# Kernel optimization log

Hardware: AMD Instinct MI355X
Metric: run time of the kernel (lower is better)

The kernel has to match this reference:

```python
import jax, jax.numpy as jnp
import numpy as np

HEADS = 8
NEG = -1e9
EPS = 1e-9


def setup_inputs() -> dict:
    key = jax.random.key(0)
    ks = jax.random.split(key, 24)
    N, D, E = 2048, 512, 64
    s = 0.02
    inp = {
        "xyz": jax.random.normal(ks[0], (N, 3), jnp.float32),
        "str_feat": jax.random.normal(ks[1], (N, D), jnp.float32),
        "esm_feat": jax.random.normal(ks[2], (N, E), jnp.float32),
        "y_hat": jax.random.uniform(ks[3], (N, 1), jnp.float32),
        "distance_mask": jax.random.randint(ks[4], (N, N), 0, 2, jnp.int32),
        "t": jnp.ones((1,), jnp.float32),
        "band_width": jnp.ones((1,), jnp.float32),
        "max_iter": 5,
        # main projections (torch Linear layout: y = x @ W.T + b)
        "Wq": jax.random.normal(ks[5], (D, D), jnp.float32) * s,
        "bq": jnp.zeros((D,), jnp.float32),
        "Wk": jax.random.normal(ks[6], (D, D), jnp.float32) * s,
        "bk": jnp.zeros((D,), jnp.float32),
        "Wv": jax.random.normal(ks[7], (D, D), jnp.float32) * s,
        "bv": jnp.zeros((D,), jnp.float32),
        "Wo": jax.random.normal(ks[8], (D, D), jnp.float32) * s,
        "bo": jnp.zeros((D,), jnp.float32),
        # esm projections (computed in the original forward but unused downstream)
        "Weq": jax.random.normal(ks[9], (E, E), jnp.float32) * s,
        "beq": jnp.zeros((E,), jnp.float32),
        "Wek": jax.random.normal(ks[10], (E, E), jnp.float32) * s,
        "bek": jnp.zeros((E,), jnp.float32),
        "Wev": jax.random.normal(ks[11], (E, E), jnp.float32) * s,
        "bev": jnp.zeros((E,), jnp.float32),
        "Weo": jax.random.normal(ks[12], (E, E), jnp.float32) * s,
        "beo": jnp.zeros((E,), jnp.float32),
    }
    return inp


def reference(xyz, str_feat, esm_feat, y_hat, distance_mask, t, band_width, max_iter,
              Wq, bq, Wk, bk, Wv, bv, Wo, bo,
              Weq, beq, Wek, bek, Wev, bev, Weo, beo):
    N, D = str_feat.shape
    h = HEADS
    dh = D // h

    q = str_feat @ Wq.T + bq
    k = str_feat @ Wk.T + bk
    v = str_feat @ Wv.T + bv
    # esm projections: computed in the original forward but never used (dead code; DCE'd under jit)
    _esm_q = esm_feat @ Weq.T + beq
    _esm_k = esm_feat @ Wek.T + bek
    _esm_v = esm_feat @ Wev.T + bev

    # [h, N, dh]
    qh = q.reshape(N, h, dh).transpose(1, 0, 2)
    kh = k.reshape(N, h, dh).transpose(1, 0, 2)
    vh = v.reshape(N, h, dh).transpose(1, 0, 2)

    scores = jnp.einsum('hnd,hmd->hnm', qh, kh) / jnp.sqrt(jnp.asarray(dh, qh.dtype))
    mask = (distance_mask > 0)[None]              # [1, N, N]
    yw = y_hat[:, 0][None, :]                     # [1, N] per-target weight
    inv_two_bw2 = 1.0 / (2.0 * band_width[0] ** 2)
    temp = t[0]

    def step(carry, _):
        xyz_c, _x = carry
        # squared pairwise distances via the expanded form (avoids [N,N,3])
        sq = jnp.sum(xyz_c * xyz_c, axis=-1)
        d2 = sq[:, None] + sq[None, :] - 2.0 * (xyz_c @ xyz_c.T)
        kern = jnp.exp(-d2 * inv_two_bw2)          # [N, N] band-width kernel
        logits = scores / temp + jnp.log(kern * yw + EPS)[None]
        logits = jnp.where(mask, logits, NEG)
        attn = jax.nn.softmax(logits, axis=-1)     # [h, N, N]
        xyz_new = jnp.einsum('nm,md->nd', attn.mean(0), xyz_c)  # mean-shift step
        x_new = jnp.einsum('hnm,hmd->hnd', attn, vh)            # [h, N, dh]
        return (xyz_new, x_new), None

    (xyz_out, xh), _ = jax.lax.scan(step, (xyz, jnp.zeros_like(vh)), None, length=max_iter)
    x = xh.transpose(1, 0, 2).reshape(N, D)
    out = x @ Wo.T + bo
    return xyz_out, out
```

## Files before the change

### kernel.cpp

```cpp
#include <hip/hip_runtime.h>


typedef __attribute__((ext_vector_type(8))) short bf16x8;
typedef __attribute__((ext_vector_type(4))) float f32x4;

__device__ __forceinline__ unsigned short f2bf(float f) {
    unsigned int u = __float_as_uint(f);
    u += 0x7fff + ((u >> 16) & 1);
    return (unsigned short)(u >> 16);
}
__device__ __forceinline__ float bf2f(unsigned short u) {
    return __uint_as_float((unsigned int)u << 16);
}

union EU { bf16x8 v; unsigned short u[8]; };

__global__ __launch_bounds__(256)
void conv_all(const float* __restrict__ strf,
              const float* __restrict__ Wq, const float* __restrict__ Wk,
              const float* __restrict__ Wv, const float* __restrict__ Wo,
              const int* __restrict__ dmask,
              unsigned short* __restrict__ sA, unsigned short* __restrict__ sW,
              unsigned char* __restrict__ mby)
{
    const long base = (long)(blockIdx.x * 256 + threadIdx.x) * 8;
    if (base >= 2097152) {
        const long rel = base - 2097152;
        int4 a = *reinterpret_cast<const int4*>(dmask + rel);
        int4 b = *reinterpret_cast<const int4*>(dmask + rel + 4);
        unsigned long long p = 0;
        p |= (a.x > 0) ? 0x01ULL : 0;  p |= (a.y > 0) ? 0x0100ULL : 0;
        p |= (a.z > 0) ? 0x010000ULL : 0;  p |= (a.w > 0) ? 0x01000000ULL : 0;
        p |= (b.x > 0) ? 0x0100000000ULL : 0;  p |= (b.y > 0) ? 0x010000000000ULL : 0;
        p |= (b.z > 0) ? 0x01000000000000ULL : 0;  p |= (b.w > 0) ? 0x0100000000000000ULL : 0;
        *reinterpret_cast<unsigned long long*>(mby + rel) = p;
        return;
    }
    const float* src;
    unsigned short* dst;
    if (base < 1048576) {
        src = strf + base; dst = sA + base;
    } else {
        const long rel = base - 1048576;
        const int seg = (int)(rel >> 18);
        const long off = rel & 262143;
        const float* Ws[4] = {Wq, Wk, Wv, Wo};
        src = Ws[seg] + off;
        dst = sW + (long)seg * 262144 + off;
    }
    float4 a = *reinterpret_cast<const float4*>(src);
    float4 b = *reinterpret_cast<const float4*>(src + 4);
    EU o;
    o.u[0] = f2bf(a.x); o.u[1] = f2bf(a.y); o.u[2] = f2bf(a.z); o.u[3] = f2bf(a.w);
    o.u[4] = f2bf(b.x); o.u[5] = f2bf(b.y); o.u[6] = f2bf(b.z); o.u[7] = f2bf(b.w);
    *reinterpret_cast<bf16x8*>(dst) = o.v;
}

__global__ __launch_bounds__(256)
void qkv_mfma(const unsigned short* __restrict__ sA,
              const unsigned short* __restrict__ sW,
              const float* __restrict__ bq, const float* __restrict__ bk,
              const float* __restrict__ bv,
              unsigned short* __restrict__ qh, unsigned short* __restrict__ kh,
              unsigned short* __restrict__ vT)
{
    const int z  = blockIdx.z;
    const int bx = blockIdx.x;
    const int by = blockIdx.y;
    const int tid = threadIdx.x;
    const int wv = tid >> 6;
    const int lane = tid & 63;
    const int row  = lane & 15;
    const int koct = (lane >> 4) * 8;
    const int n0 = bx * 64;

    const unsigned short* Ap = sA + (long)(n0 + wv * 16 + row) * 512;
    const unsigned short* Bp = sW + (long)z * 262144 + (long)(by * 64 + row) * 512;

    f32x4 acc[4] = {};
#pragma unroll
    for (int k0 = 0; k0 < 512; k0 += 32) {
        bf16x8 a = *reinterpret_cast<const bf16x8*>(Ap + k0 + koct);
#pragma unroll
        for (int t = 0; t < 4; t++) {
            bf16x8 b = *reinterpret_cast<const bf16x8*>(Bp + (long)(t * 16) * 512 + k0 + koct);
            acc[t] = __builtin_amdgcn_mfma_f32_16x16x32_bf16(a, b, acc[t], 0, 0, 0);
        }
    }

    if (z == 2) {
        const int rbase = n0 + wv * 16 + (lane >> 4) * 4;
#pragma unroll
        for (int t = 0; t < 4; t++) {
            const int d = by * 64 + t * 16 + (lane & 15);
            const float bb = bv[d];
            ushort4 o;
            o.x = f2bf(acc[t][0] + bb); o.y = f2bf(acc[t][1] + bb);
            o.z = f2bf(acc[t][2] + bb); o.w = f2bf(acc[t][3] + bb);
            *reinterpret_cast<ushort4*>(vT + (long)d * 2048 + rbase) = o;
        }
        return;
    }

    __shared__ float ls[64][68];
    const int lrb = wv * 16 + (lane >> 4) * 4;
    const int lcb = lane & 15;
#pragma unroll
    for (int t = 0; t < 4; t++)
#pragma unroll
        for (int r = 0; r < 4; r++)
            ls[lrb + r][t * 16 + lcb] = acc[t][r];
    __syncthreads();

    const float* bias = (z == 0) ? bq : bk;
    unsigned short* dst = (z == 0) ? qh : kh;
    const int r2 = tid >> 2;
    const int c2 = (tid & 3) * 16;
    float sv[16];
#pragma unroll
    for (int j = 0; j < 4; j++) {
        float4 s = *reinterpret_cast<const float4*>(&ls[r2][c2 + j * 4]);
        float4 bb = *reinterpret_cast<const float4*>(bias + by * 64 + c2 + j * 4);
        sv[j*4+0] = s.x + bb.x; sv[j*4+1] = s.y + bb.y;
        sv[j*4+2] = s.z + bb.z; sv[j*4+3] = s.w + bb.w;
    }
    EU o0, o1;
#pragma unroll
    for (int j = 0; j < 8; j++) { o0.u[j] = f2bf(sv[j]); o1.u[j] = f2bf(sv[8 + j]); }
    unsigned short* dp = dst + (long)(n0 + r2) * 512 + by * 64 + c2;
    *reinterpret_cast<bf16x8*>(dp)     = o0.v;
    *reinterpret_cast<bf16x8*>(dp + 8) = o1.v;
}

__global__ __launch_bounds__(256)
void scores_rows(const unsigned short* __restrict__ qh,
                 const unsigned short* __restrict__ kh,
                 const unsigned char* __restrict__ mby,
                 const float* __restrict__ tptr,
                 unsigned short* __restrict__ Ebf)
{
    const int h  = blockIdx.y;
    const int n0 = blockIdx.x * 16;
    const int tid = threadIdx.x;
    const int wv = tid >> 6;
    const int lane = tid & 63;
    const float scale = 1.0f / (8.0f * tptr[0]);

    __shared__ unsigned short lsb[4][16][260];

    const int arow = lane & 15;
    const int koct = (lane >> 4) * 8;
    const unsigned short* Aq = qh + (long)(n0 + arow) * 512 + h * 64;
    const bf16x8 aq0 = *reinterpret_cast<const bf16x8*>(Aq + koct);
    const bf16x8 aq1 = *reinterpret_cast<const bf16x8*>(Aq + 32 + koct);

    const int lr = (lane >> 4) * 4;
    const int lc = lane & 15;
    const int rlo = lane >> 5;
    const int cch = lane & 31;

#pragma unroll
    for (int half = 0; half < 2; half++) {
        const int mbase = wv * 512 + half * 256;
#pragma unroll
        for (int mt = 0; mt < 16; mt++) {
            const unsigned short* Bk = kh + (long)(mbase + mt * 16 + arow) * 512 + h * 64;
            bf16x8 b0 = *reinterpret_cast<const bf16x8*>(Bk + koct);
            bf16x8 b1 = *reinterpret_cast<const bf16x8*>(Bk + 32 + koct);
            f32x4 c = {};
            c = __builtin_amdgcn_mfma_f32_16x16x32_bf16(aq0, b0, c, 0, 0, 0);
            c = __builtin_amdgcn_mfma_f32_16x16x32_bf16(aq1, b1, c, 0, 0, 0);
#pragma unroll
            for (int r = 0; r < 4; r++)
                lsb[wv][lr + r][mt * 16 + lc] = f2bf(__expf(c[r] * scale));
        }
#pragma unroll
        for (int rp = 0; rp < 8; rp++) {
            const int row = rp * 2 + rlo;
            const int gn = n0 + row;
            const int m = mbase + cch * 8;
            EU e;
            e.v = *reinterpret_cast<const bf16x8*>(&lsb[wv][row][cch * 8]);
            unsigned long long mk =
                *reinterpret_cast<const unsigned long long*>(mby + (long)gn * 2048 + m);
            EU o;
#pragma unroll
            for (int j = 0; j < 8; j++)
                o.u[j] = ((mk >> (8 * j)) & 0xff) ? e.u[j] : (unsigned short)0;
            *reinterpret_cast<bf16x8*>(Ebf + ((long)h * 2048 + gn) * 2048 + m) = o.v;
        }
    }
}

__global__ __launch_bounds__(256)
void ms_iter(const unsigned short* __restrict__ Ebf,
             const float* __restrict__ xyz_src,
             float* __restrict__ xyz_dst,
             const float* __restrict__ y_hat,
             const float* __restrict__ bwp,
             unsigned short* __restrict__ gbf,
             float* __restrict__ invzb,
             int wlast)
{
    const int n = blockIdx.x;
    const int tid = threadIdx.x;
    const int lane = tid & 63;
    const int wave = tid >> 6;
    const int m0 = tid * 8;

    __shared__ unsigned short Es[8][4][512];
    __shared__ float red[64];

    {
        const unsigned short* gp = Ebf + (long)n * 2048 + wave * 512 + lane * 8;
#pragma unroll
        for (int h = 0; h < 8; h++) {
            __builtin_amdgcn_global_load_lds(
                (const __attribute__((address_space(1))) unsigned int*)(gp + (long)h * 4194304),
                (__attribute__((address_space(3))) unsigned int*)&Es[h][wave][0],
                16, 0, 0);
        }
    }

    const float bw = bwp[0];
    const float c2k = 1.0f / (2.0f * bw * bw);
    const float xn = xyz_src[n * 3 + 0];
    const float yn = xyz_src[n * 3 + 1];
    const float zn = xyz_src[n * 3 + 2];
    const float sqn = xn * xn + yn * yn + zn * zn;

    float mx[8], my[8], mz[8];
    {
        const float4* xp = reinterpret_cast<const float4*>(xyz_src + (long)m0 * 3);
        float4 a = xp[0], b = xp[1], c = xp[2], d = xp[3], e = xp[4], f = xp[5];
        mx[0]=a.x; my[0]=a.y; mz[0]=a.z;  mx[1]=a.w; my[1]=b.x; mz[1]=b.y;
        mx[2]=b.z; my[2]=b.w; mz[2]=c.x;  mx[3]=c.y; my[3]=c.z; mz[3]=c.w;
        mx[4]=d.x; my[4]=d.y; mz[4]=d.z;  mx[5]=d.w; my[5]=e.x; mz[5]=e.y;
        mx[6]=e.z; my[6]=e.w; mz[6]=f.x;  mx[7]=f.y; my[7]=f.z; mz[7]=f.w;
    }
    float4 yh0 = *reinterpret_cast<const float4*>(y_hat + m0);
    float4 yh1 = *reinterpret_cast<const float4*>(y_hat + m0 + 4);
    float yh[8] = {yh0.x, yh0.y, yh0.z, yh0.w, yh1.x, yh1.y, yh1.z, yh1.w};

    float g[8];
#pragma unroll
    for (int j = 0; j < 8; j++) {
        const float d2 = sqn + (mx[j]*mx[j] + my[j]*my[j] + mz[j]*mz[j])
                       - 2.0f * (xn*mx[j] + yn*my[j] + zn*mz[j]);
        g[j] = __expf(-d2 * c2k) * yh[j] + 1e-9f;
    }

    __syncthreads();

    EU E[8];
#pragma unroll
    for (int h = 0; h < 8; h++)
        E[h].v = *reinterpret_cast<const bf16x8*>(&Es[h][wave][lane * 8]);

    float z[8];
#pragma unroll
    for (int h = 0; h < 8; h++) {
        float zz = 0.f;
#pragma unroll
        for (int j = 0; j < 8; j++) zz += bf2f(E[h].u[j]) * g[j];
        z[h] = zz;
    }

#pragma unroll
    for (int h = 0; h < 8; h++) {
        float v = z[h];
#pragma unroll
        for (int off = 32; off > 0; off >>= 1) v += __shfl_down(v, off, 64);
        if (lane == 0) red[wave * 8 + h] = v;
    }
    __syncthreads();
    if (tid < 8) {
        const float s = red[tid] + red[8 + tid] + red[16 + tid] + red[24 + tid];
        const float iz = 1.0f / s;
        red[32 + tid] = iz;
        if (wlast) invzb[tid * 2048 + n] = iz;
    }
    __syncthreads();
    float invz[8];
#pragma unroll
    for (int h = 0; h < 8; h++) invz[h] = red[32 + h];

    float ax = 0.f, ay = 0.f, az = 0.f;
#pragma unroll
    for (int j = 0; j < 8; j++) {
        float w = 0.f;
#pragma unroll
        for (int h = 0; h < 8; h++) w += bf2f(E[h].u[j]) * invz[h];
        w *= 0.125f * g[j];
        ax += w * mx[j]; ay += w * my[j]; az += w * mz[j];
    }
    if (wlast) {
        EU og;
#pragma unroll
        for (int j = 0; j < 8; j++) og.u[j] = f2bf(g[j]);
        *reinterpret_cast<bf16x8*>(gbf + (long)n * 2048 + m0) = og.v;
    }

    float v3[3] = {ax, ay, az};
#pragma unroll
    for (int c = 0; c < 3; c++) {
        float v = v3[c];
#pragma unroll
        for (int off = 32; off > 0; off >>= 1) v += __shfl_down(v, off, 64);
        if (lane == 0) red[40 + c * 4 + wave] = v;
    }
    __syncthreads();
    if (tid < 3) {
        xyz_dst[n * 3 + tid] = red[40 + tid * 4 + 0] + red[40 + tid * 4 + 1] +
                               red[40 + tid * 4 + 2] + red[40 + tid * 4 + 3];
    }
}

__global__ __launch_bounds__(256)
void av_mfma(const unsigned short* __restrict__ Ebf,
             const unsigned short* __restrict__ gbf,
             const unsigned short* __restrict__ vT,
             float* __restrict__ P)
{
    const int h  = blockIdx.z;
    const int s  = blockIdx.y;
    const int bx = blockIdx.x;
    const int tid = threadIdx.x;
    const int wv = tid >> 6;
    const int lane = tid & 63;
    const int n0 = bx * 64;
    const int kc = s * 512;

    __shared__ unsigned short As[64][132];

    const int mrow = lane & 15;
    const int koct = (lane >> 4) * 8;
    const int srow = tid >> 4;
    const int skk  = (tid & 15) * 8;

    f32x4 acc[4] = {};
    for (int kt = 0; kt < 4; kt++) {
        const int kb = kc + kt * 128;
        __syncthreads();
#pragma unroll
        for (int l = 0; l < 4; l++) {
            const int row = l * 16 + srow;
            EU e, gg;
            e.v  = *reinterpret_cast<const bf16x8*>(Ebf + ((long)h * 2048 + n0 + row) * 2048 + kb + skk);
            gg.v = *reinterpret_cast<const bf16x8*>(gbf + (long)(n0 + row) * 2048 + kb + skk);
            EU a;
#pragma unroll
            for (int j = 0; j < 8; j++)
                a.u[j] = f2bf(bf2f(e.u[j]) * bf2f(gg.u[j]));
            *reinterpret_cast<bf16x8*>(&As[row][skk]) = a.v;
        }
        __syncthreads();
#pragma unroll
        for (int k2 = 0; k2 < 128; k2 += 32) {
            bf16x8 a = *reinterpret_cast<const bf16x8*>(&As[wv * 16 + mrow][k2 + koct]);
#pragma unroll
            for (int t = 0; t < 4; t++) {
                bf16x8 b = *reinterpret_cast<const bf16x8*>(
                    vT + ((long)h * 64 + t * 16 + mrow) * 2048 + kb + k2 + koct);
                acc[t] = __builtin_amdgcn_mfma_f32_16x16x32_bf16(a, b, acc[t], 0, 0, 0);
            }
        }
    }

    float* Pp = P + (long)s * 1048576;
    const int rbase = n0 + wv * 16 + (lane >> 4) * 4;
    const int dcol = lane & 15;
#pragma unroll
    for (int t = 0; t < 4; t++)
#pragma unroll
        for (int r = 0; r < 4; r++)
            Pp[(long)(rbase + r) * 512 + h * 64 + t * 16 + dcol] = acc[t][r];
}

__global__ __launch_bounds__(256)
void av_red(const float* __restrict__ P, const float* __restrict__ invzb,
            unsigned short* __restrict__ xc)
{
    const long idx = (long)(blockIdx.x * 256 + threadIdx.x) * 8;
    const int n = (int)(idx >> 9);
    const int d0 = (int)(idx & 511);
    const float iz = invzb[(d0 >> 6) * 2048 + n];
    float s[8] = {};
#pragma unroll
    for (int p = 0; p < 4; p++) {
        const float* pp = P + (long)p * 1048576 + idx;
        float4 a = *reinterpret_cast<const float4*>(pp);
        float4 b = *reinterpret_cast<const float4*>(pp + 4);
        s[0] += a.x; s[1] += a.y; s[2] += a.z; s[3] += a.w;
        s[4] += b.x; s[5] += b.y; s[6] += b.z; s[7] += b.w;
    }
    EU o;
#pragma unroll
    for (int j = 0; j < 8; j++) o.u[j] = f2bf(s[j] * iz);
    *reinterpret_cast<bf16x8*>(xc + idx) = o.v;
}

__global__ __launch_bounds__(256)
void out_mfma(const unsigned short* __restrict__ xc,
              const unsigned short* __restrict__ sW,
              const float* __restrict__ bo,
              float* __restrict__ out)
{
    const int bx = blockIdx.x;
    const int by = blockIdx.y;
    const int wv = threadIdx.x >> 6;
    const int lane = threadIdx.x & 63;
    const int row  = lane & 15;
    const int koct = (lane >> 4) * 8;
    const int n0 = bx * 64;

    const unsigned short* Ap = xc + (long)(n0 + wv * 16 + row) * 512;
    const unsigned short* Bp = sW + 3L * 262144 + (long)(by * 64 + row) * 512;

    f32x4 acc[4] = {};
#pragma unroll
    for (int k0 = 0; k0 < 512; k0 += 32) {
        bf16x8 a = *reinterpret_cast<const bf16x8*>(Ap + k0 + koct);
#pragma unroll
        for (int t = 0; t < 4; t++) {
            bf16x8 b = *reinterpret_cast<const bf16x8*>(Bp + (long)(t * 16) * 512 + k0 + koct);
            acc[t] = __builtin_amdgcn_mfma_f32_16x16x32_bf16(a, b, acc[t], 0, 0, 0);
        }
    }

    const int rbase = n0 + wv * 16 + (lane >> 4) * 4;
    const int dcol = lane & 15;
#pragma unroll
    for (int t = 0; t < 4; t++) {
        const int col = by * 64 + t * 16 + dcol;
        const float bb = bo[col];
#pragma unroll
        for (int r = 0; r < 4; r++)
            out[(long)(rbase + r) * 512 + col] = acc[t][r] + bb;
    }
}

extern "C" void kernel_launch(void* const* d_in, const int* in_sizes, int n_in,
                              void* d_out, int out_size, void* d_ws, size_t ws_size,
                              hipStream_t stream)
{
    (void)in_sizes; (void)n_in; (void)out_size; (void)ws_size;

    const float* xyz   = (const float*)d_in[0];
    const float* strf  = (const float*)d_in[1];
    const float* yhat  = (const float*)d_in[3];
    const int*   dmask = (const int*)d_in[4];
    const float* tptr  = (const float*)d_in[5];
    const float* bwptr = (const float*)d_in[6];
    const float* Wq = (const float*)d_in[8];
    const float* bq = (const float*)d_in[9];
    const float* Wk = (const float*)d_in[10];
    const float* bk = (const float*)d_in[11];
    const float* Wv = (const float*)d_in[12];
    const float* bv = (const float*)d_in[13];
    const float* Wo = (const float*)d_in[14];
    const float* bo = (const float*)d_in[15];
    float* outp = (float*)d_out;

    char* wsb = (char*)d_ws;
    float* Ppart         = (float*)(wsb);
    unsigned short* xc   = (unsigned short*)(wsb + (16L << 20));
    unsigned short* sA   = (unsigned short*)(wsb + (18L << 20));
    unsigned short* sW   = (unsigned short*)(wsb + (20L << 20));
    unsigned short* qh   = (unsigned short*)(wsb + (22L << 20));
    unsigned short* kh   = (unsigned short*)(wsb + (24L << 20));
    unsigned short* vT   = (unsigned short*)(wsb + (26L << 20));
    float* xyzA          = (float*)(wsb + (28L << 20));
    float* xyzB          = xyzA + 8192;
    unsigned char* mby   = (unsigned char*)(wsb + (30L << 20));
    unsigned short* Ebf  = (unsigned short*)(wsb + (34L << 20));
    unsigned short* gbf  = (unsigned short*)(wsb + (98L << 20));
    float* invzb         = (float*)(wsb + (106L << 20));

    dim3 blk(256, 1, 1);

    conv_all<<<dim3(3072), blk, 0, stream>>>(strf, Wq, Wk, Wv, Wo, dmask, sA, sW, mby);
    qkv_mfma<<<dim3(32, 8, 3), blk, 0, stream>>>(sA, sW, bq, bk, bv, qh, kh, vT);

    scores_rows<<<dim3(128, 8), blk, 0, stream>>>(qh, kh, mby, tptr, Ebf);

    const float* src = xyz;
    float* dsts[5] = {xyzA, xyzB, xyzA, xyzB, outp};
    for (int it = 0; it < 5; it++) {
        ms_iter<<<dim3(2048), blk, 0, stream>>>(Ebf, src, dsts[it], yhat, bwptr,
                                                gbf, invzb, it == 4 ? 1 : 0);
        src = dsts[it];
    }

    av_mfma<<<dim3(32, 4, 8), blk, 0, stream>>>(Ebf, gbf, vT, Ppart);
    av_red<<<dim3(512), blk, 0, stream>>>(Ppart, invzb, xc);
    out_mfma<<<dim3(32, 8), blk, 0, stream>>>(xc, sW, bo, outp + 6144);
}
```

Measured before the change: 315.1 us.

## Split score kernel over grid z and double-buffer rows in mean-shift kernel

The score kernel now launches a third grid dimension for the two column halves, which doubles the block count, and it preloads the mask words before the MFMA loop. The mean-shift iteration kernel handles four query rows per block instead of one. It double-buffers the per-head E rows into LDS through async global_load_lds, controlled by explicit vmcnt waits, and computes per-column squared norms once. This is meant to hide global load latency and amortise xyz/y_hat loads. The cost is fewer blocks (512) and hand-written waitcnt/barrier code, which is fragile and could hurt occupancy.

```diff
diff --git a/kernel.cpp b/kernel.cpp
--- a/kernel.cpp
+++ b/kernel.cpp
@@ -139,10 +139,11 @@
                  const float* __restrict__ tptr,
                  unsigned short* __restrict__ Ebf)
 {
-    const int h  = blockIdx.y;
-    const int n0 = blockIdx.x * 16;
-    const int tid = threadIdx.x;
-    const int wv = tid >> 6;
+    const int h    = blockIdx.y;
+    const int n0   = blockIdx.x * 16;
+    const int half = blockIdx.z;
+    const int tid  = threadIdx.x;
+    const int wv   = tid >> 6;
     const int lane = tid & 63;
     const float scale = 1.0f / (8.0f * tptr[0]);
 
@@ -150,45 +151,47 @@
 
     const int arow = lane & 15;
     const int koct = (lane >> 4) * 8;
+    const int mbase = wv * 512 + half * 256;
+    const int rlo = lane >> 5;
+    const int cch = lane & 31;
+
+    unsigned long long mk[8];
+#pragma unroll
+    for (int rp = 0; rp < 8; rp++)
+        mk[rp] = *reinterpret_cast<const unsigned long long*>(
+            mby + (long)(n0 + rp * 2 + rlo) * 2048 + mbase + cch * 8);
+
     const unsigned short* Aq = qh + (long)(n0 + arow) * 512 + h * 64;
     const bf16x8 aq0 = *reinterpret_cast<const bf16x8*>(Aq + koct);
     const bf16x8 aq1 = *reinterpret_cast<const bf16x8*>(Aq + 32 + koct);
 
     const int lr = (lane >> 4) * 4;
     const int lc = lane & 15;
-    const int rlo = lane >> 5;
-    const int cch = lane & 31;
-
-#pragma unroll
-    for (int half = 0; half < 2; half++) {
-        const int mbase = wv * 512 + half * 256;
-#pragma unroll
-        for (int mt = 0; mt < 16; mt++) {
-            const unsigned short* Bk = kh + (long)(mbase + mt * 16 + arow) * 512 + h * 64;
-            bf16x8 b0 = *reinterpret_cast<const bf16x8*>(Bk + koct);
-            bf16x8 b1 = *reinterpret_cast<const bf16x8*>(Bk + 32 + koct);
-            f32x4 c = {};
-            c = __builtin_amdgcn_mfma_f32_16x16x32_bf16(aq0, b0, c, 0, 0, 0);
-            c = __builtin_amdgcn_mfma_f32_16x16x32_bf16(aq1, b1, c, 0, 0, 0);
-#pragma unroll
-            for (int r = 0; r < 4; r++)
-                lsb[wv][lr + r][mt * 16 + lc] = f2bf(__expf(c[r] * scale));
-        }
-#pragma unroll
-        for (int rp = 0; rp < 8; rp++) {
-            const int row = rp * 2 + rlo;
-            const int gn = n0 + row;
-            const int m = mbase + cch * 8;
-            EU e;
-            e.v = *reinterpret_cast<const bf16x8*>(&lsb[wv][row][cch * 8]);
-            unsigned long long mk =
-                *reinterpret_cast<const unsigned long long*>(mby + (long)gn * 2048 + m);
-            EU o;
-#pragma unroll
-            for (int j = 0; j < 8; j++)
-                o.u[j] = ((mk >> (8 * j)) & 0xff) ? e.u[j] : (unsigned short)0;
-            *reinterpret_cast<bf16x8*>(Ebf + ((long)h * 2048 + gn) * 2048 + m) = o.v;
-        }
+
+#pragma unroll
+    for (int mt = 0; mt < 16; mt++) {
+        const unsigned short* Bk = kh + (long)(mbase + mt * 16 + arow) * 512 + h * 64;
+        bf16x8 b0 = *reinterpret_cast<const bf16x8*>(Bk + koct);
+        bf16x8 b1 = *reinterpret_cast<const bf16x8*>(Bk + 32 + koct);
+        f32x4 c = {};
+        c = __builtin_amdgcn_mfma_f32_16x16x32_bf16(aq0, b0, c, 0, 0, 0);
+        c = __builtin_amdgcn_mfma_f32_16x16x32_bf16(aq1, b1, c, 0, 0, 0);
+#pragma unroll
+        for (int r = 0; r < 4; r++)
+            lsb[wv][lr + r][mt * 16 + lc] = f2bf(__expf(c[r] * scale));
+    }
+
+#pragma unroll
+    for (int rp = 0; rp < 8; rp++) {
+        const int row = rp * 2 + rlo;
+        EU e;
+        e.v = *reinterpret_cast<const bf16x8*>(&lsb[wv][row][cch * 8]);
+        EU o;
+#pragma unroll
+        for (int j = 0; j < 8; j++)
+            o.u[j] = ((mk[rp] >> (8 * j)) & 0xff) ? e.u[j] : (unsigned short)0;
+        *reinterpret_cast<bf16x8*>(
+            Ebf + ((long)h * 2048 + n0 + row) * 2048 + mbase + cch * 8) = o.v;
     }
 }
 
@@ -202,34 +205,34 @@
              float* __restrict__ invzb,
              int wlast)
 {
-    const int n = blockIdx.x;
-    const int tid = threadIdx.x;
+    const int tid  = threadIdx.x;
     const int lane = tid & 63;
     const int wave = tid >> 6;
-    const int m0 = tid * 8;
-
-    __shared__ unsigned short Es[8][4][512];
+    const int m0   = tid * 8;
+    const int nb   = blockIdx.x * 4;
+
+    __shared__ unsigned short Es[2][8][4][512];
     __shared__ float red[64];
 
-    {
-        const unsigned short* gp = Ebf + (long)n * 2048 + wave * 512 + lane * 8;
-#pragma unroll
-        for (int h = 0; h < 8; h++) {
-            __builtin_amdgcn_global_load_lds(
-                (const __attribute__((address_space(1))) unsigned int*)(gp + (long)h * 4194304),
-                (__attribute__((address_space(3))) unsigned int*)&Es[h][wave][0],
-                16, 0, 0);
-        }
-    }
+    const unsigned short* gp0 = Ebf + (long)nb * 2048 + wave * 512 + lane * 8;
+
+#pragma unroll
+    for (int h = 0; h < 8; h++)
+        __builtin_amdgcn_global_load_lds(
+            (const __attribute__((address_space(1))) unsigned int*)(gp0 + (long)h * 4194304),
+            (__attribute__((address_space(3))) unsigned int*)&Es[0][h][wave][0],
+            16, 0, 0);
 
     const float bw = bwp[0];
     const float c2k = 1.0f / (2.0f * bw * bw);
-    const float xn = xyz_src[n * 3 + 0];
-    const float yn = xyz_src[n * 3 + 1];
-    const float zn = xyz_src[n * 3 + 2];
-    const float sqn = xn * xn + yn * yn + zn * zn;
-
-    float mx[8], my[8], mz[8];
+    float4 rA = *reinterpret_cast<const float4*>(xyz_src + nb * 3);
+    float4 rB = *reinterpret_cast<const float4*>(xyz_src + nb * 3 + 4);
+    float4 rC = *reinterpret_cast<const float4*>(xyz_src + nb * 3 + 8);
+    const float rx[4] = {rA.x, rA.w, rB.z, rC.y};
+    const float ry[4] = {rA.y, rB.x, rB.w, rC.z};
+    const float rz[4] = {rA.z, rB.y, rC.x, rC.w};
+
+    float mx[8], my[8], mz[8], sqm[8], yh[8];
     {
         const float4* xp = reinterpret_cast<const float4*>(xyz_src + (long)m0 * 3);
         float4 a = xp[0], b = xp[1], c = xp[2], d = xp[3], e = xp[4], f = xp[5];
@@ -237,82 +240,112 @@
         mx[2]=b.z; my[2]=b.w; mz[2]=c.x;  mx[3]=c.y; my[3]=c.z; mz[3]=c.w;
         mx[4]=d.x; my[4]=d.y; mz[4]=d.z;  mx[5]=d.w; my[5]=e.x; mz[5]=e.y;
         mx[6]=e.z; my[6]=e.w; mz[6]=f.x;  mx[7]=f.y; my[7]=f.z; mz[7]=f.w;
-    }
-    float4 yh0 = *reinterpret_cast<const float4*>(y_hat + m0);
-    float4 yh1 = *reinterpret_cast<const float4*>(y_hat + m0 + 4);
-    float yh[8] = {yh0.x, yh0.y, yh0.z, yh0.w, yh1.x, yh1.y, yh1.z, yh1.w};
-
-    float g[8];
-#pragma unroll
-    for (int j = 0; j < 8; j++) {
-        const float d2 = sqn + (mx[j]*mx[j] + my[j]*my[j] + mz[j]*mz[j])
-                       - 2.0f * (xn*mx[j] + yn*my[j] + zn*mz[j]);
-        g[j] = __expf(-d2 * c2k) * yh[j] + 1e-9f;
-    }
-
-    __syncthreads();
-
-    EU E[8];
+        float4 y0 = *reinterpret_cast<const float4*>(y_hat + m0);
+        float4 y1 = *reinterpret_cast<const float4*>(y_hat + m0 + 4);
+        yh[0]=y0.x; yh[1]=y0.y; yh[2]=y0.z; yh[3]=y0.w;
+        yh[4]=y1.x; yh[5]=y1.y; yh[6]=y1.z; yh[7]=y1.w;
+#pragma unroll
+        for (int j = 0; j < 8; j++)
+            sqm[j] = mx[j]*mx[j] + my[j]*my[j] + mz[j]*mz[j];
+    }
+
 #pragma unroll
     for (int h = 0; h < 8; h++)
-        E[h].v = *reinterpret_cast<const bf16x8*>(&Es[h][wave][lane * 8]);
-
-    float z[8];
-#pragma unroll
-    for (int h = 0; h < 8; h++) {
-        float zz = 0.f;
-#pragma unroll
-        for (int j = 0; j < 8; j++) zz += bf2f(E[h].u[j]) * g[j];
-        z[h] = zz;
-    }
-
-#pragma unroll
-    for (int h = 0; h < 8; h++) {
-        float v = z[h];
-#pragma unroll
-        for (int off = 32; off > 0; off >>= 1) v += __shfl_down(v, off, 64);
-        if (lane == 0) red[wave * 8 + h] = v;
-    }
-    __syncthreads();
-    if (tid < 8) {
-        const float s = red[tid] + red[8 + tid] + red[16 + tid] + red[24 + tid];
-        const float iz = 1.0f / s;
-        red[32 + tid] = iz;
-        if (wlast) invzb[tid * 2048 + n] = iz;
-    }
-    __syncthreads();
-    float invz[8];
-#pragma unroll
-    for (int h = 0; h < 8; h++) invz[h] = red[32 + h];
-
-    float ax = 0.f, ay = 0.f, az = 0.f;
-#pragma unroll
-    for (int j = 0; j < 8; j++) {
-        float w = 0.f;
-#pragma unroll
-        for (int h = 0; h < 8; h++) w += bf2f(E[h].u[j]) * invz[h];
-        w *= 0.125f * g[j];
-        ax += w * mx[j]; ay += w * my[j]; az += w * mz[j];
-    }
-    if (wlast) {
-        EU og;
-#pragma unroll
-        for (int j = 0; j < 8; j++) og.u[j] = f2bf(g[j]);
-        *reinterpret_cast<bf16x8*>(gbf + (long)n * 2048 + m0) = og.v;
-    }
-
-    float v3[3] = {ax, ay, az};
-#pragma unroll
-    for (int c = 0; c < 3; c++) {
-        float v = v3[c];
-#pragma unroll
-        for (int off = 32; off > 0; off >>= 1) v += __shfl_down(v, off, 64);
-        if (lane == 0) red[40 + c * 4 + wave] = v;
-    }
-    __syncthreads();
-    if (tid < 3) {
-        xyz_dst[n * 3 + tid] = red[40 + tid * 4 + 0] + red[40 + tid * 4 + 1] +
-                               red[40 + tid * 4 + 2] + red[40 + tid * 4 + 3];
+        __builtin_amdgcn_global_load_lds(
+            (const __attribute__((address_space(1))) unsigned int*)(gp0 + 2048 + (long)h * 4194304),
+            (__attribute__((address_space(3))) unsigned int*)&Es[1][h][wave][0],
+            16, 0, 0);
+
+#pragma unroll
+    for (int r = 0; r < 4; r++) {
+        const int n = nb + r;
+        const float xn = rx[r], yn = ry[r], zn = rz[r];
+        const float sqn = xn*xn + yn*yn + zn*zn;
+        float g[8];
+#pragma unroll
+        for (int j = 0; j < 8; j++) {
+            const float d2 = sqn + sqm[j] - 2.0f * (xn*mx[j] + yn*my[j] + zn*mz[j]);
+            g[j] = __expf(-d2 * c2k) * yh[j] + 1e-9f;
+        }
+
+        if (r < 3) asm volatile("s_waitcnt vmcnt(8)" ::: "memory");
+        else       asm volatile("s_waitcnt vmcnt(0)" ::: "memory");
+
+        EU E[8];
+#pragma unroll
+        for (int h = 0; h < 8; h++)
+            E[h].v = *reinterpret_cast<const bf16x8*>(&Es[r & 1][h][wave][lane * 8]);
+        asm volatile("s_waitcnt lgkmcnt(0)" ::: "memory");
+
+        if (r < 2) {
+            const unsigned short* gp = gp0 + (long)(r + 2) * 2048;
+#pragma unroll
+            for (int h = 0; h < 8; h++)
+                __builtin_amdgcn_global_load_lds(
+                    (const __attribute__((address_space(1))) unsigned int*)(gp + (long)h * 4194304),
+                    (__attribute__((address_space(3))) unsigned int*)&Es[r & 1][h][wave][0],
+                    16, 0, 0);
+        }
+
+        float z8[8];
+#pragma unroll
+        for (int h = 0; h < 8; h++) {
+            float zz = 0.f;
+#pragma unroll
+            for (int j = 0; j < 8; j++) zz += bf2f(E[h].u[j]) * g[j];
+            z8[h] = zz;
+        }
+#pragma unroll
+        for (int h = 0; h < 8; h++) {
+            float v = z8[h];
+#pragma unroll
+            for (int off = 32; off > 0; off >>= 1) v += __shfl_down(v, off, 64);
+            if (lane == 0) red[wave * 8 + h] = v;
+        }
+        asm volatile("s_waitcnt lgkmcnt(0)" ::: "memory");
+        __builtin_amdgcn_s_barrier();
+        if (tid < 8) {
+            const float s = red[tid] + red[8 + tid] + red[16 + tid] + red[24 + tid];
+            const float iz = 1.0f / s;
+            red[32 + tid] = iz;
+            if (wlast) invzb[tid * 2048 + n] = iz;
+        }
+        asm volatile("s_waitcnt lgkmcnt(0)" ::: "memory");
+        __builtin_amdgcn_s_barrier();
+        float invz[8];
+#pragma unroll
+        for (int h = 0; h < 8; h++) invz[h] = red[32 + h];
+
+        float ax = 0.f, ay = 0.f, az = 0.f;
+#pragma unroll
+        for (int j = 0; j < 8; j++) {
+            float w = 0.f;
+#pragma unroll
+            for (int h = 0; h < 8; h++) w += bf2f(E[h].u[j]) * invz[h];
+            w *= 0.125f * g[j];
+            ax += w * mx[j]; ay += w * my[j]; az += w * mz[j];
+        }
+        if (wlast) {
+            EU og;
+#pragma unroll
+            for (int j = 0; j < 8; j++) og.u[j] = f2bf(g[j]);
+            *reinterpret_cast<bf16x8*>(gbf + (long)n * 2048 + m0) = og.v;
+        }
+
+        float v3[3] = {ax, ay, az};
+#pragma unroll
+        for (int c = 0; c < 3; c++) {
+            float v = v3[c];
+#pragma unroll
+            for (int off = 32; off > 0; off >>= 1) v += __shfl_down(v, off, 64);
+            if (lane == 0) red[40 + c * 4 + wave] = v;
+        }
+        asm volatile("s_waitcnt lgkmcnt(0)" ::: "memory");
+        __builtin_amdgcn_s_barrier();
+        if (tid < 3) {
+            xyz_dst[n * 3 + tid] = red[40 + tid * 4 + 0] + red[40 + tid * 4 + 1] +
+                                   red[40 + tid * 4 + 2] + red[40 + tid * 4 + 3];
+        }
     }
 }
 
@@ -482,13 +515,13 @@
     conv_all<<<dim3(3072), blk, 0, stream>>>(strf, Wq, Wk, Wv, Wo, dmask, sA, sW, mby);
     qkv_mfma<<<dim3(32, 8, 3), blk, 0, stream>>>(sA, sW, bq, bk, bv, qh, kh, vT);
 
-    scores_rows<<<dim3(128, 8), blk, 0, stream>>>(qh, kh, mby, tptr, Ebf);
+    scores_rows<<<dim3(128, 8, 2), blk, 0, stream>>>(qh, kh, mby, tptr, Ebf);
 
     const float* src = xyz;
     float* dsts[5] = {xyzA, xyzB, xyzA, xyzB, outp};
     for (int it = 0; it < 5; it++) {
-        ms_iter<<<dim3(2048), blk, 0, stream>>>(Ebf, src, dsts[it], yhat, bwptr,
-                                                gbf, invzb, it == 4 ? 1 : 0);
+        ms_iter<<<dim3(512), blk, 0, stream>>>(Ebf, src, dsts[it], yhat, bwptr,
+                                               gbf, invzb, it == 4 ? 1 : 0);
         src = dsts[it];
     }
 
```

After: 349.3 us. +10.8%, slower.

## Recompute attention scores on the fly instead of materializing bf16 score tensor

Applied to the files above, without the earlier changes.

Drops the precomputed masked exp(QK^T) bf16 tensor, which was written once and then read on every mean-shift iteration and again in the AV pass. Each iteration now recomputes QK^T with MFMA inside a fused kernel, `ms_zS`. That kernel folds in the distance kernel and the mask and writes per-slice partial sums of z and the weighted xyz. A small `ms_fin` kernel then reduces those partials into the new coordinates and the inverse normalisers. The AV kernel likewise recomputes the scores and combines them with a separately generated `gbf` kernel matrix. This trades several passes over a large HBM buffer for repeated matrix-core compute and exp work, plus more kernel launches per iteration.

```diff
diff --git a/kernel.cpp b/kernel.cpp
--- a/kernel.cpp
+++ b/kernel.cpp
@@ -133,193 +133,217 @@
 }
 
 __global__ __launch_bounds__(256)
-void scores_rows(const unsigned short* __restrict__ qh,
-                 const unsigned short* __restrict__ kh,
-                 const unsigned char* __restrict__ mby,
-                 const float* __restrict__ tptr,
-                 unsigned short* __restrict__ Ebf)
-{
-    const int h  = blockIdx.y;
+void ms_zS(const unsigned short* __restrict__ qh,
+           const unsigned short* __restrict__ kh,
+           const unsigned char* __restrict__ mby,
+           const float* __restrict__ xyz_src,
+           const float* __restrict__ y_hat,
+           const float* __restrict__ tptr,
+           const float* __restrict__ bwp,
+           float* __restrict__ Pzs)
+{
     const int n0 = blockIdx.x * 16;
-    const int tid = threadIdx.x;
-    const int wv = tid >> 6;
-    const int lane = tid & 63;
-    const float scale = 1.0f / (8.0f * tptr[0]);
-
-    __shared__ unsigned short lsb[4][16][260];
-
-    const int arow = lane & 15;
-    const int koct = (lane >> 4) * 8;
-    const unsigned short* Aq = qh + (long)(n0 + arow) * 512 + h * 64;
-    const bf16x8 aq0 = *reinterpret_cast<const bf16x8*>(Aq + koct);
-    const bf16x8 aq1 = *reinterpret_cast<const bf16x8*>(Aq + 32 + koct);
-
-    const int lr = (lane >> 4) * 4;
-    const int lc = lane & 15;
-    const int rlo = lane >> 5;
-    const int cch = lane & 31;
-
-#pragma unroll
-    for (int half = 0; half < 2; half++) {
-        const int mbase = wv * 512 + half * 256;
-#pragma unroll
-        for (int mt = 0; mt < 16; mt++) {
-            const unsigned short* Bk = kh + (long)(mbase + mt * 16 + arow) * 512 + h * 64;
-            bf16x8 b0 = *reinterpret_cast<const bf16x8*>(Bk + koct);
-            bf16x8 b1 = *reinterpret_cast<const bf16x8*>(Bk + 32 + koct);
-            f32x4 c = {};
-            c = __builtin_amdgcn_mfma_f32_16x16x32_bf16(aq0, b0, c, 0, 0, 0);
-            c = __builtin_amdgcn_mfma_f32_16x16x32_bf16(aq1, b1, c, 0, 0, 0);
-#pragma unroll
-            for (int r = 0; r < 4; r++)
-                lsb[wv][lr + r][mt * 16 + lc] = f2bf(__expf(c[r] * scale));
-        }
-#pragma unroll
-        for (int rp = 0; rp < 8; rp++) {
-            const int row = rp * 2 + rlo;
-            const int gn = n0 + row;
-            const int m = mbase + cch * 8;
-            EU e;
-            e.v = *reinterpret_cast<const bf16x8*>(&lsb[wv][row][cch * 8]);
-            unsigned long long mk =
-                *reinterpret_cast<const unsigned long long*>(mby + (long)gn * 2048 + m);
-            EU o;
-#pragma unroll
-            for (int j = 0; j < 8; j++)
-                o.u[j] = ((mk >> (8 * j)) & 0xff) ? e.u[j] : (unsigned short)0;
-            *reinterpret_cast<bf16x8*>(Ebf + ((long)h * 2048 + gn) * 2048 + m) = o.v;
-        }
-    }
-}
-
-__global__ __launch_bounds__(256)
-void ms_iter(const unsigned short* __restrict__ Ebf,
-             const float* __restrict__ xyz_src,
-             float* __restrict__ xyz_dst,
-             const float* __restrict__ y_hat,
-             const float* __restrict__ bwp,
-             unsigned short* __restrict__ gbf,
-             float* __restrict__ invzb,
-             int wlast)
-{
-    const int n = blockIdx.x;
+    const int mc = blockIdx.y * 512;
     const int tid = threadIdx.x;
     const int lane = tid & 63;
-    const int wave = tid >> 6;
-    const int m0 = tid * 8;
-
-    __shared__ unsigned short Es[8][4][512];
-    __shared__ float red[64];
-
-    {
-        const unsigned short* gp = Ebf + (long)n * 2048 + wave * 512 + lane * 8;
-#pragma unroll
-        for (int h = 0; h < 8; h++) {
-            __builtin_amdgcn_global_load_lds(
-                (const __attribute__((address_space(1))) unsigned int*)(gp + (long)h * 4194304),
-                (__attribute__((address_space(3))) unsigned int*)&Es[h][wave][0],
-                16, 0, 0);
-        }
-    }
-
+    const int wv = tid >> 6;
+    const int q = lane >> 4;
+    const int mcol = lane & 15;
+    const int arow = lane & 15;
+    const int koct = q * 8;
+
+    __shared__ float sxn[16], syn[16], szn[16], ssn[16];
+    __shared__ float smx[512], smy[512], smz[512], ssq[512], syh[512];
+
+    if (tid < 16) {
+        const float x = xyz_src[(n0 + tid) * 3 + 0];
+        const float y = xyz_src[(n0 + tid) * 3 + 1];
+        const float z = xyz_src[(n0 + tid) * 3 + 2];
+        sxn[tid] = x; syn[tid] = y; szn[tid] = z; ssn[tid] = x*x + y*y + z*z;
+    }
+#pragma unroll
+    for (int k = 0; k < 2; k++) {
+        const int ml = tid * 2 + k;
+        const int mg = mc + ml;
+        const float x = xyz_src[mg * 3 + 0];
+        const float y = xyz_src[mg * 3 + 1];
+        const float z = xyz_src[mg * 3 + 2];
+        smx[ml] = x; smy[ml] = y; smz[ml] = z;
+        ssq[ml] = x*x + y*y + z*z;
+        syh[ml] = y_hat[mg];
+    }
+    __syncthreads();
+
+    const float scale = 1.0f / (8.0f * tptr[0]);
     const float bw = bwp[0];
     const float c2k = 1.0f / (2.0f * bw * bw);
-    const float xn = xyz_src[n * 3 + 0];
-    const float yn = xyz_src[n * 3 + 1];
-    const float zn = xyz_src[n * 3 + 2];
-    const float sqn = xn * xn + yn * yn + zn * zn;
-
-    float mx[8], my[8], mz[8];
-    {
-        const float4* xp = reinterpret_cast<const float4*>(xyz_src + (long)m0 * 3);
-        float4 a = xp[0], b = xp[1], c = xp[2], d = xp[3], e = xp[4], f = xp[5];
-        mx[0]=a.x; my[0]=a.y; mz[0]=a.z;  mx[1]=a.w; my[1]=b.x; mz[1]=b.y;
-        mx[2]=b.z; my[2]=b.w; mz[2]=c.x;  mx[3]=c.y; my[3]=c.z; mz[3]=c.w;
-        mx[4]=d.x; my[4]=d.y; mz[4]=d.z;  mx[5]=d.w; my[5]=e.x; mz[5]=e.y;
-        mx[6]=e.z; my[6]=e.w; mz[6]=f.x;  mx[7]=f.y; my[7]=f.z; mz[7]=f.w;
-    }
-    float4 yh0 = *reinterpret_cast<const float4*>(y_hat + m0);
-    float4 yh1 = *reinterpret_cast<const float4*>(y_hat + m0 + 4);
-    float yh[8] = {yh0.x, yh0.y, yh0.z, yh0.w, yh1.x, yh1.y, yh1.z, yh1.w};
-
-    float g[8];
-#pragma unroll
-    for (int j = 0; j < 8; j++) {
-        const float d2 = sqn + (mx[j]*mx[j] + my[j]*my[j] + mz[j]*mz[j])
-                       - 2.0f * (xn*mx[j] + yn*my[j] + zn*mz[j]);
-        g[j] = __expf(-d2 * c2k) * yh[j] + 1e-9f;
-    }
-
+
+    float xn[4], yn[4], zn[4], sq4[4];
+#pragma unroll
+    for (int r = 0; r < 4; r++) {
+        xn[r] = sxn[q * 4 + r]; yn[r] = syn[q * 4 + r];
+        zn[r] = szn[q * 4 + r]; sq4[r] = ssn[q * 4 + r];
+    }
+
+    const int mwave = mc + wv * 128;
+    const int slice = blockIdx.y * 4 + wv;
+
+#pragma unroll
+    for (int hh = 0; hh < 8; hh += 4) {
+        bf16x8 aq0[4], aq1[4];
+#pragma unroll
+        for (int h4 = 0; h4 < 4; h4++) {
+            const unsigned short* Ap = qh + (long)(n0 + arow) * 512 + (hh + h4) * 64;
+            aq0[h4] = *reinterpret_cast<const bf16x8*>(Ap + koct);
+            aq1[h4] = *reinterpret_cast<const bf16x8*>(Ap + 32 + koct);
+        }
+        float zc[4][4] = {};
+        float Sx[4][4] = {}, Sy[4][4] = {}, Sz[4][4] = {};
+
+#pragma unroll
+        for (int mt = 0; mt < 8; mt++) {
+            const int ml = wv * 128 + mt * 16 + mcol;
+            const float xm = smx[ml], ym = smy[ml], zm = smz[ml];
+            const float sm = ssq[ml], yhm = syh[ml];
+            float gm[4];
+#pragma unroll
+            for (int r = 0; r < 4; r++) {
+                const float d2 = sq4[r] + sm
+                               - 2.0f * (xn[r]*xm + yn[r]*ym + zn[r]*zm);
+                const float gv = __expf(-d2 * c2k) * yhm + 1e-9f;
+                const unsigned char mk =
+                    mby[(long)(n0 + q * 4 + r) * 2048 + mc + wv * 128 + mt * 16 + mcol];
+                gm[r] = mk ? gv : 0.0f;
+            }
+#pragma unroll
+            for (int h4 = 0; h4 < 4; h4++) {
+                const unsigned short* Bk =
+                    kh + (long)(mwave + mt * 16 + arow) * 512 + (hh + h4) * 64;
+                bf16x8 b0 = *reinterpret_cast<const bf16x8*>(Bk + koct);
+                bf16x8 b1 = *reinterpret_cast<const bf16x8*>(Bk + 32 + koct);
+                f32x4 c = {};
+                c = __builtin_amdgcn_mfma_f32_16x16x32_bf16(aq0[h4], b0, c, 0, 0, 0);
+                c = __builtin_amdgcn_mfma_f32_16x16x32_bf16(aq1[h4], b1, c, 0, 0, 0);
+#pragma unroll
+                for (int r = 0; r < 4; r++) {
+                    const float t = __expf(c[r] * scale) * gm[r];
+                    zc[h4][r] += t;
+                    Sx[h4][r] = fmaf(t, xm, Sx[h4][r]);
+                    Sy[h4][r] = fmaf(t, ym, Sy[h4][r]);
+                    Sz[h4][r] = fmaf(t, zm, Sz[h4][r]);
+                }
+            }
+        }
+
+#pragma unroll
+        for (int d = 1; d < 16; d <<= 1) {
+#pragma unroll
+            for (int h4 = 0; h4 < 4; h4++)
+#pragma unroll
+                for (int r = 0; r < 4; r++) {
+                    zc[h4][r] += __shfl_xor(zc[h4][r], d, 64);
+                    Sx[h4][r] += __shfl_xor(Sx[h4][r], d, 64);
+                    Sy[h4][r] += __shfl_xor(Sy[h4][r], d, 64);
+                    Sz[h4][r] += __shfl_xor(Sz[h4][r], d, 64);
+                }
+        }
+        if (mcol == 0) {
+#pragma unroll
+            for (int h4 = 0; h4 < 4; h4++)
+#pragma unroll
+                for (int r = 0; r < 4; r++) {
+                    float4 o = make_float4(zc[h4][r], Sx[h4][r], Sy[h4][r], Sz[h4][r]);
+                    *reinterpret_cast<float4*>(
+                        Pzs + (((long)slice * 2048 + n0 + q * 4 + r) * 8 + hh + h4) * 4) = o;
+                }
+        }
+    }
+}
+
+__global__ __launch_bounds__(256)
+void ms_fin(const float* __restrict__ Pzs,
+            float* __restrict__ xyz_dst,
+            float* __restrict__ invzb,
+            int wlast)
+{
+    const int gid = blockIdx.x * 256 + threadIdx.x;
+    const int n = gid >> 3;
+    const int h = gid & 7;
+    const float4* P4 = reinterpret_cast<const float4*>(Pzs);
+    float z = 0.f, sx = 0.f, sy = 0.f, sz = 0.f;
+#pragma unroll
+    for (int s = 0; s < 16; s++) {
+        float4 p = P4[((long)s * 2048 + n) * 8 + h];
+        z += p.x; sx += p.y; sy += p.z; sz += p.w;
+    }
+    const float iz = 1.0f / z;
+    if (wlast) invzb[h * 2048 + n] = iz;
+    float cx = iz * sx, cy = iz * sy, cz = iz * sz;
+#pragma unroll
+    for (int d = 1; d < 8; d <<= 1) {
+        cx += __shfl_xor(cx, d, 64);
+        cy += __shfl_xor(cy, d, 64);
+        cz += __shfl_xor(cz, d, 64);
+    }
+    if (h == 0) {
+        xyz_dst[n * 3 + 0] = cx * 0.125f;
+        xyz_dst[n * 3 + 1] = cy * 0.125f;
+        xyz_dst[n * 3 + 2] = cz * 0.125f;
+    }
+}
+
+__global__ __launch_bounds__(256)
+void g_kern(const float* __restrict__ xyz4,
+            const float* __restrict__ y_hat,
+            const unsigned char* __restrict__ mby,
+            const float* __restrict__ bwp,
+            unsigned short* __restrict__ gbf)
+{
+    const int mc = blockIdx.x * 512;
+    const int n0 = blockIdx.y * 8;
+    const int tid = threadIdx.x;
+
+    __shared__ float sxn[8], syn[8], szn[8], ssn[8];
+    if (tid < 8) {
+        const float x = xyz4[(n0 + tid) * 3 + 0];
+        const float y = xyz4[(n0 + tid) * 3 + 1];
+        const float z = xyz4[(n0 + tid) * 3 + 2];
+        sxn[tid] = x; syn[tid] = y; szn[tid] = z; ssn[tid] = x*x + y*y + z*z;
+    }
     __syncthreads();
 
-    EU E[8];
-#pragma unroll
-    for (int h = 0; h < 8; h++)
-        E[h].v = *reinterpret_cast<const bf16x8*>(&Es[h][wave][lane * 8]);
-
-    float z[8];
-#pragma unroll
-    for (int h = 0; h < 8; h++) {
-        float zz = 0.f;
-#pragma unroll
-        for (int j = 0; j < 8; j++) zz += bf2f(E[h].u[j]) * g[j];
-        z[h] = zz;
-    }
-
-#pragma unroll
-    for (int h = 0; h < 8; h++) {
-        float v = z[h];
-#pragma unroll
-        for (int off = 32; off > 0; off >>= 1) v += __shfl_down(v, off, 64);
-        if (lane == 0) red[wave * 8 + h] = v;
-    }
-    __syncthreads();
-    if (tid < 8) {
-        const float s = red[tid] + red[8 + tid] + red[16 + tid] + red[24 + tid];
-        const float iz = 1.0f / s;
-        red[32 + tid] = iz;
-        if (wlast) invzb[tid * 2048 + n] = iz;
-    }
-    __syncthreads();
-    float invz[8];
-#pragma unroll
-    for (int h = 0; h < 8; h++) invz[h] = red[32 + h];
-
-    float ax = 0.f, ay = 0.f, az = 0.f;
-#pragma unroll
-    for (int j = 0; j < 8; j++) {
-        float w = 0.f;
-#pragma unroll
-        for (int h = 0; h < 8; h++) w += bf2f(E[h].u[j]) * invz[h];
-        w *= 0.125f * g[j];
-        ax += w * mx[j]; ay += w * my[j]; az += w * mz[j];
-    }
-    if (wlast) {
-        EU og;
-#pragma unroll
-        for (int j = 0; j < 8; j++) og.u[j] = f2bf(g[j]);
-        *reinterpret_cast<bf16x8*>(gbf + (long)n * 2048 + m0) = og.v;
-    }
-
-    float v3[3] = {ax, ay, az};
-#pragma unroll
-    for (int c = 0; c < 3; c++) {
-        float v = v3[c];
-#pragma unroll
-        for (int off = 32; off > 0; off >>= 1) v += __shfl_down(v, off, 64);
-        if (lane == 0) red[40 + c * 4 + wave] = v;
-    }
-    __syncthreads();
-    if (tid < 3) {
-        xyz_dst[n * 3 + tid] = red[40 + tid * 4 + 0] + red[40 + tid * 4 + 1] +
-                               red[40 + tid * 4 + 2] + red[40 + tid * 4 + 3];
-    }
-}
-
-__global__ __launch_bounds__(256)
-void av_mfma(const unsigned short* __restrict__ Ebf,
+    const float bw = bwp[0];
+    const float c2k = 1.0f / (2.0f * bw * bw);
+    const int m0 = mc + tid * 2;
+
+    const float x0 = xyz4[m0 * 3 + 0], y0 = xyz4[m0 * 3 + 1], z0 = xyz4[m0 * 3 + 2];
+    const float x1 = xyz4[m0 * 3 + 3], y1 = xyz4[m0 * 3 + 4], z1 = xyz4[m0 * 3 + 5];
+    const float s0 = x0*x0 + y0*y0 + z0*z0;
+    const float s1 = x1*x1 + y1*y1 + z1*z1;
+    const float yh0 = y_hat[m0], yh1 = y_hat[m0 + 1];
+
+#pragma unroll
+    for (int r = 0; r < 8; r++) {
+        const float xr = sxn[r], yr = syn[r], zr = szn[r], sr = ssn[r];
+        const float d20 = sr + s0 - 2.0f * (xr*x0 + yr*y0 + zr*z0);
+        const float d21 = sr + s1 - 2.0f * (xr*x1 + yr*y1 + zr*z1);
+        const float g0 = __expf(-d20 * c2k) * yh0 + 1e-9f;
+        const float g1 = __expf(-d21 * c2k) * yh1 + 1e-9f;
+        const unsigned short mk2 = *reinterpret_cast<const unsigned short*>(
+            mby + (long)(n0 + r) * 2048 + m0);
+        ushort2 o;
+        o.x = (mk2 & 0xff) ? f2bf(g0) : (unsigned short)0;
+        o.y = (mk2 >> 8)   ? f2bf(g1) : (unsigned short)0;
+        *reinterpret_cast<ushort2*>(gbf + (long)(n0 + r) * 2048 + m0) = o;
+    }
+}
+
+__global__ __launch_bounds__(256)
+void av_mfma(const unsigned short* __restrict__ qh,
+             const unsigned short* __restrict__ kh,
              const unsigned short* __restrict__ gbf,
              const unsigned short* __restrict__ vT,
+             const float* __restrict__ tptr,
              float* __restrict__ P)
 {
     const int h  = blockIdx.z;
@@ -330,51 +354,77 @@
     const int lane = tid & 63;
     const int n0 = bx * 64;
     const int kc = s * 512;
+    const int q = lane >> 4;
+    const int mcol = lane & 15;
+    const int arow = lane & 15;
+    const int koct = q * 8;
 
     __shared__ unsigned short As[64][132];
-
-    const int mrow = lane & 15;
-    const int koct = (lane >> 4) * 8;
-    const int srow = tid >> 4;
-    const int skk  = (tid & 15) * 8;
+    __shared__ unsigned short gs[64][128];
+
+    const float scale = 1.0f / (8.0f * tptr[0]);
+
+    const unsigned short* Ap = qh + (long)(n0 + wv * 16 + arow) * 512 + h * 64;
+    const bf16x8 aq0 = *reinterpret_cast<const bf16x8*>(Ap + koct);
+    const bf16x8 aq1 = *reinterpret_cast<const bf16x8*>(Ap + 32 + koct);
 
     f32x4 acc[4] = {};
     for (int kt = 0; kt < 4; kt++) {
         const int kb = kc + kt * 128;
-        __syncthreads();
-#pragma unroll
-        for (int l = 0; l < 4; l++) {
-            const int row = l * 16 + srow;
-            EU e, gg;
-            e.v  = *reinterpret_cast<const bf16x8*>(Ebf + ((long)h * 2048 + n0 + row) * 2048 + kb + skk);
-            gg.v = *reinterpret_cast<const bf16x8*>(gbf + (long)(n0 + row) * 2048 + kb + skk);
-            EU a;
-#pragma unroll
-            for (int j = 0; j < 8; j++)
-                a.u[j] = f2bf(bf2f(e.u[j]) * bf2f(gg.u[j]));
-            *reinterpret_cast<bf16x8*>(&As[row][skk]) = a.v;
-        }
-        __syncthreads();
+
+#pragma unroll
+        for (int i = 0; i < 4; i++) {
+            __builtin_amdgcn_global_load_lds(
+                (const __attribute__((address_space(1))) unsigned int*)(
+                    gbf + (long)(n0 + wv * 16 + i * 4 + (lane >> 4)) * 2048
+                        + kb + (lane & 15) * 8),
+                (__attribute__((address_space(3))) unsigned int*)&gs[wv * 16 + i * 4][0],
+                16, 0, 0);
+        }
+
+        f32x4 c[8];
+#pragma unroll
+        for (int mt = 0; mt < 8; mt++) {
+            const unsigned short* Bk =
+                kh + (long)(kb + mt * 16 + arow) * 512 + h * 64;
+            bf16x8 b0 = *reinterpret_cast<const bf16x8*>(Bk + koct);
+            bf16x8 b1 = *reinterpret_cast<const bf16x8*>(Bk + 32 + koct);
+            f32x4 cc = {};
+            cc = __builtin_amdgcn_mfma_f32_16x16x32_bf16(aq0, b0, cc, 0, 0, 0);
+            cc = __builtin_amdgcn_mfma_f32_16x16x32_bf16(aq1, b1, cc, 0, 0, 0);
+            c[mt] = cc;
+        }
+
+        asm volatile("s_waitcnt vmcnt(0)" ::: "memory");
+
+#pragma unroll
+        for (int mt = 0; mt < 8; mt++)
+#pragma unroll
+            for (int r = 0; r < 4; r++) {
+                const float e = __expf(c[mt][r] * scale);
+                const unsigned short gv = gs[wv * 16 + q * 4 + r][mt * 16 + mcol];
+                As[wv * 16 + q * 4 + r][mt * 16 + mcol] = f2bf(e * bf2f(gv));
+            }
+
 #pragma unroll
         for (int k2 = 0; k2 < 128; k2 += 32) {
-            bf16x8 a = *reinterpret_cast<const bf16x8*>(&As[wv * 16 + mrow][k2 + koct]);
+            bf16x8 a = *reinterpret_cast<const bf16x8*>(&As[wv * 16 + arow][k2 + koct]);
 #pragma unroll
             for (int t = 0; t < 4; t++) {
                 bf16x8 b = *reinterpret_cast<const bf16x8*>(
-                    vT + ((long)h * 64 + t * 16 + mrow) * 2048 + kb + k2 + koct);
+                    vT + ((long)h * 64 + t * 16 + arow) * 2048 + kb + k2 + koct);
                 acc[t] = __builtin_amdgcn_mfma_f32_16x16x32_bf16(a, b, acc[t], 0, 0, 0);
             }
         }
     }
 
     float* Pp = P + (long)s * 1048576;
-    const int rbase = n0 + wv * 16 + (lane >> 4) * 4;
-    const int dcol = lane & 15;
+    const int rbase = n0 + wv * 16 + q * 4;
 #pragma unroll
     for (int t = 0; t < 4; t++)
 #pragma unroll
         for (int r = 0; r < 4; r++)
-            Pp[(long)(rbase + r) * 512 + h * 64 + t * 16 + dcol] = acc[t][r];
+            Pp[(long)(rbase + r) * 512 + h * 64 + t * 16 + mcol] = acc[t][r];
 }
 
 __global__ __launch_bounds__(256)
@@ -473,26 +523,25 @@
     float* xyzA          = (float*)(wsb + (28L << 20));
     float* xyzB          = xyzA + 8192;
     unsigned char* mby   = (unsigned char*)(wsb + (30L << 20));
-    unsigned short* Ebf  = (unsigned short*)(wsb + (34L << 20));
-    unsigned short* gbf  = (unsigned short*)(wsb + (98L << 20));
-    float* invzb         = (float*)(wsb + (106L << 20));
+    float* Pzs           = (float*)(wsb + (34L << 20));
+    unsigned short* gbf  = (unsigned short*)(wsb + (40L << 20));
+    float* invzb         = (float*)(wsb + (50L << 20));
 
     dim3 blk(256, 1, 1);
 
     conv_all<<<dim3(3072), blk, 0, stream>>>(strf, Wq, Wk, Wv, Wo, dmask, sA, sW, mby);
     qkv_mfma<<<dim3(32, 8, 3), blk, 0, stream>>>(sA, sW, bq, bk, bv, qh, kh, vT);
-
-    scores_rows<<<dim3(128, 8), blk, 0, stream>>>(qh, kh, mby, tptr, Ebf);
 
     const float* src = xyz;
     float* dsts[5] = {xyzA, xyzB, xyzA, xyzB, outp};
     for (int it = 0; it < 5; it++) {
-        ms_iter<<<dim3(2048), blk, 0, stream>>>(Ebf, src, dsts[it], yhat, bwptr,
-                                                gbf, invzb, it == 4 ? 1 : 0);
+        ms_zS<<<dim3(128, 4), blk, 0, stream>>>(qh, kh, mby, src, yhat, tptr, bwptr, Pzs);
+        ms_fin<<<dim3(64), blk, 0, stream>>>(Pzs, dsts[it], invzb, it == 4 ? 1 : 0);
         src = dsts[it];
     }
 
-    av_mfma<<<dim3(32, 4, 8), blk, 0, stream>>>(Ebf, gbf, vT, Ppart);
+    g_kern<<<dim3(4, 256), blk, 0, stream>>>(xyzB, yhat, mby, bwptr, gbf);
+    av_mfma<<<dim3(32, 4, 8), blk, 0, stream>>>(qh, kh, gbf, vT, tptr, Ppart);
     av_red<<<dim3(512), blk, 0, stream>>>(Ppart, invzb, xc);
     out_mfma<<<dim3(32, 8), blk, 0, stream>>>(xc, sW, bo, outp + 6144);
 }
```

Result: slower. 512.3 us (+62.6%).
